# Kernel optimization log

Hardware: AMD Instinct MI355X
Metric: run time of the kernel (lower is better)

Reference implementation:

```python
import jax, jax.numpy as jnp
import numpy as np

# NSA hyperparams (match init_kwargs)
D_BLK = 64    # d: block stride
L_CMP = 64    # compression block length (== d -> non-overlapping blocks)
L_SLC = 64    # selection block length (== l_cmp == d -> P_slc = P_cmp)
BQ = 64       # block_size_q
TOPK = 16     # slc_top_k
WL, WR = 512, 0  # sliding window (left, right)


def _nsa_forward(q, k, v, w_k, b_k, w_v, b_v, w_gate, b_gate, seqlen):
    S, qh, dim = q.shape
    kv = k.shape[1]
    H = qh // kv
    b = S // seqlen          # number of equal-length packed sequences
    s = seqlen
    scale = dim ** -0.5
    f32 = jnp.float32

    # [b, s, kv, H, e]: q head g*H+h belongs to kv head g (repeat_interleave layout)
    q5 = q.reshape(b, s, kv, H, dim)
    k3 = k.reshape(b, s, kv, dim)
    v3 = v.reshape(b, s, kv, dim)

    # ---- block compression (extract_blocks + cmp_linear over block length) ----
    n_blk = s // D_BLK
    kb = k.reshape(b, n_blk, D_BLK, kv, dim)
    vb = v.reshape(b, n_blk, D_BLK, kv, dim)
    K_cmp = jnp.einsum('bntke,t->bnke', kb, w_k) + b_k[0]
    V_cmp = jnp.einsum('bntke,t->bnke', vb, w_v) + b_v[0]

    # ---- compressed attention (per sequence, fp32 softmax) ----
    sc = jnp.einsum('bqkhe,bnke->bkhqn', q5, K_cmp).astype(f32) * scale
    P = jax.nn.softmax(sc, axis=-1)
    out_cmp = jnp.einsum('bkhqn,bnke->bqkhe', P.astype(q.dtype), V_cmp)

    # ---- selection scores: pool P over q-blocks and GQA groups, then top-k ----
    nqb = s // BQ
    pooled = P.reshape(b, kv, H, nqb, BQ, n_blk).sum(axis=(2, 4))  # [b,kv,nqb,n_blk]
    idx = jax.lax.top_k(pooled, TOPK)[1]                            # [b,kv,nqb,TOPK]

    # gather selected K/V blocks (shared by all queries in a q-block / GQA group)
    kb2 = jnp.transpose(kb, (0, 3, 1, 2, 4))  # [b,kv,n_blk,l,e]
    vb2 = jnp.transpose(vb, (0, 3, 1, 2, 4))
    gather = jax.vmap(jax.vmap(lambda blocks, i: blocks[i]))
    K_sel = gather(kb2, idx)  # [b,kv,nqb,TOPK,l,e]
    V_sel = gather(vb2, idx)

    # ---- selected-block attention ----
    qblk = q5.reshape(b, nqb, BQ, kv, H, dim)
    sc2 = jnp.einsum('bnckhe,bkntle->bkhnctl', qblk, K_sel).astype(f32) * scale
    sc2 = sc2.reshape(b, kv, H, nqb, BQ, TOPK * L_SLC)
    P2 = jax.nn.softmax(sc2, axis=-1).astype(q.dtype)
    out_slc = jnp.einsum('bkhncm,bknme->bnckhe', P2,
                         V_sel.reshape(b, kv, nqb, TOPK * L_SLC, dim))
    out_slc = out_slc.reshape(b, s, kv, H, dim)

    # ---- sliding-window attention (window_size=(WL, WR), non-causal flag) ----
    sw = jnp.einsum('bikhe,bjke->bkhij', q5, k3).astype(f32) * scale
    i = jnp.arange(s)[:, None]
    j = jnp.arange(s)[None, :]
    valid = (j >= i - WL) & (j <= i + WR)
    sw = jnp.where(valid, sw, -jnp.inf)
    Pw = jax.nn.softmax(sw, axis=-1).astype(q.dtype)
    out_win = jnp.einsum('bkhij,bjke->bikhe', Pw, v3)

    # ---- gated fusion of the three branches ----
    gate = jax.nn.sigmoid(jnp.einsum('bqkhe,ec->bqkhc', q5, w_gate) + b_gate)
    out = (gate[..., 0:1] * out_cmp
           + gate[..., 1:2] * out_slc
           + gate[..., 2:3] * out_win)
    return out.reshape(S, qh, dim)


def setup_inputs() -> dict:
    key = jax.random.key(0)
    ks = jax.random.split(key, 9)
    S, qh, kvh, dim = 4096, 8, 2, 128
    inp = {
        'q': jax.random.normal(ks[0], (S, qh, dim), jnp.float32),
        'k': jax.random.normal(ks[1], (S, kvh, dim), jnp.float32),
        'v': jax.random.normal(ks[2], (S, kvh, dim), jnp.float32),
        'w_k': jax.random.normal(ks[3], (L_CMP,), jnp.float32) * (L_CMP ** -0.5),
        'b_k': jax.random.normal(ks[4], (1,), jnp.float32) * 0.02,
        'w_v': jax.random.normal(ks[5], (L_CMP,), jnp.float32) * (L_CMP ** -0.5),
        'b_v': jax.random.normal(ks[6], (1,), jnp.float32) * 0.02,
        'w_gate': jax.random.normal(ks[7], (dim, 3), jnp.float32) * (dim ** -0.5),
        'b_gate': jax.random.normal(ks[8], (3,), jnp.float32) * 0.02,
        'seqlen': 2048,
    }
    return inp


def reference(q, k, v, w_k, b_k, w_v, b_v, w_gate, b_gate, seqlen):
    return _nsa_forward(q, k, v, w_k, b_k, w_v, b_v, w_gate, b_gate, seqlen)
```

## Files before the change

kernel.cpp:

```cpp
#include <hip/hip_runtime.h>
#include <hip/hip_bf16.h>


#define SEQ   2048
#define NB    2
#define KV    2
#define NH    4
#define QH    8
#define DIM   128
#define NBLK  32
#define NQB   32
#define NTOP  16
#define SCALE 0.08838834764831845f
#define QS    36
#define RS    144
#define QP    136
#define VP    72

typedef unsigned short ushort_t;
using bf16x8 = __attribute__((ext_vector_type(8))) short;
using f32x4  = __attribute__((ext_vector_type(4))) float;

__device__ __forceinline__ unsigned pkbf(float a, float b){
  union { __hip_bfloat162 h; unsigned u; } cv;
  cv.h = __float22bfloat162_rn(make_float2(a, b));
  return cv.u;
}
__device__ __forceinline__ ushort_t f2b(float f){
  union { float f; unsigned i; } x; x.f = f;
  unsigned r = x.i + 0x7fffu + ((x.i >> 16) & 1u);
  return (ushort_t)(r >> 16);
}

__global__ __launch_bounds__(256) void prep_k(
    const float* __restrict__ k, const float* __restrict__ v,
    ushort_t* __restrict__ Kb, ushort_t* __restrict__ VT)
{
  int blk = blockIdx.x;
  int db = blk & 1, rb = (blk >> 1) & 31, bbg = blk >> 6;
  int bb = bbg >> 1, g = bbg & 1;
  int tid = threadIdx.x;
  __shared__ ushort_t T[64*VP];

  for (int jj = 0; jj < 4; ++jj){
    int i = tid + jj*256;
    int r = i >> 4, ds = i & 15;
    size_t src = ((size_t)(bb*SEQ + rb*64 + r)*KV + g)*DIM + db*64 + ds*4;
    float4 kx = *(const float4*)(k + src);
    float4 vx = *(const float4*)(v + src);
    uint2 kk; kk.x = pkbf(kx.x,kx.y); kk.y = pkbf(kx.z,kx.w);
    *(uint2*)&Kb[((size_t)bbg*SEQ + rb*64 + r)*DIM + db*64 + ds*4] = kk;
    unsigned v01 = pkbf(vx.x,vx.y), v23 = pkbf(vx.z,vx.w);
    T[(ds*4+0)*VP + r] = (ushort_t)(v01 & 0xffffu);
    T[(ds*4+1)*VP + r] = (ushort_t)(v01 >> 16);
    T[(ds*4+2)*VP + r] = (ushort_t)(v23 & 0xffffu);
    T[(ds*4+3)*VP + r] = (ushort_t)(v23 >> 16);
  }
  __syncthreads();
  for (int jj = 0; jj < 4; ++jj){
    int i = tid + jj*256;
    int d = i >> 4, seg = i & 15;
    uint2 u = *(uint2*)&T[d*VP + seg*4];
    *(uint2*)&VT[((size_t)bbg*DIM + db*64 + d)*SEQ + rb*64 + seg*4] = u;
  }
}

__global__ __launch_bounds__(256) void compress_k(
    const float* __restrict__ k, const float* __restrict__ v,
    const float* __restrict__ w_k, const float* __restrict__ b_k,
    const float* __restrict__ w_v, const float* __restrict__ b_v,
    float* __restrict__ Kc, float* __restrict__ Vc)
{
  int blk = blockIdx.x;
  int dh = blk & 1;
  int n  = (blk >> 1) & 31;
  int g  = (blk >> 6) & 1;
  int bb = blk >> 7;
  int tid = threadIdx.x;

  __shared__ float wks[64], wvs[64];
  __shared__ float accK[16][64], accV[16][64];
  if (tid < 64){ wks[tid] = w_k[tid]; wvs[tid] = w_v[tid]; }
  __syncthreads();

  int r4 = tid >> 4, dq = tid & 15;
  float4 sk = {0,0,0,0}, sv = {0,0,0,0};
  for (int rr = 0; rr < 4; ++rr){
    int row = r4*4 + rr;
    size_t off = ((size_t)(bb*SEQ + n*64 + row)*KV + g)*DIM + dh*64 + dq*4;
    float4 kx = *(const float4*)(k + off);
    float4 vx = *(const float4*)(v + off);
    float a = wks[row], b = wvs[row];
    sk.x += a*kx.x; sk.y += a*kx.y; sk.z += a*kx.z; sk.w += a*kx.w;
    sv.x += b*vx.x; sv.y += b*vx.y; sv.z += b*vx.z; sv.w += b*vx.w;
  }
  *(float4*)&accK[r4][dq*4] = sk;
  *(float4*)&accV[r4][dq*4] = sv;
  __syncthreads();
  size_t obase = ((size_t)((bb*KV+g)*NBLK + n))*DIM + dh*64;
  if (tid < 64){
    float s = 0.f;
#pragma unroll
    for (int i = 0; i < 16; ++i) s += accK[i][tid];
    Kc[obase + tid] = s + b_k[0];
  } else if (tid < 128){
    int d = tid - 64;
    float s = 0.f;
#pragma unroll
    for (int i = 0; i < 16; ++i) s += accV[i][d];
    Vc[obase + d] = s + b_v[0];
  }
}

__global__ __launch_bounds__(256) void cmp_attn_k(
    const float* __restrict__ q, const float* __restrict__ Kc,
    const float* __restrict__ Vc,
    const float* __restrict__ w_gate, const float* __restrict__ b_gate,
    float* __restrict__ pooled_part, float* __restrict__ out)
{
  int blk = blockIdx.x;
  int h  = blk & 3;
  int qb = (blk >> 2) & (NQB-1);
  int g  = (blk >> 7) & 1;
  int bb = blk >> 8;
  int tid = threadIdx.x;
  int qi = tid >> 2, c = tid & 3;

  __shared__ float Ks[32*RS];
  __shared__ float Vs[32*RS];
  __shared__ float wsum[4][NBLK];

  const float4* Ksrc = (const float4*)(Kc + (size_t)(bb*KV + g) * NBLK * DIM);
  const float4* Vsrc = (const float4*)(Vc + (size_t)(bb*KV + g) * NBLK * DIM);
  for (int i = tid; i < 1024; i += 256){
    int row = i >> 5, seg = i & 31;
    int dst = row*RS + (seg>>3)*QS + (seg&7)*4;
    ((float4*)(Ks+dst))[0] = Ksrc[i];
    ((float4*)(Vs+dst))[0] = Vsrc[i];
  }
  __syncthreads();

  int row = bb*SEQ + qb*64 + qi;
  float qv[32];
  {
    const float4* q4 = (const float4*)(q + ((size_t)row*QH + g*NH + h)*DIM + c*32);
#pragma unroll
    for (int j = 0; j < 8; ++j){
      float4 u = q4[j];
      qv[4*j+0]=u.x; qv[4*j+1]=u.y; qv[4*j+2]=u.z; qv[4*j+3]=u.w;
    }
  }

  float gp = 0.f;
#pragma unroll
  for (int d = 0; d < 32; ++d) gp += qv[d]*w_gate[(c*32+d)*3 + 0];
  gp += __shfl_xor(gp, 1); gp += __shfl_xor(gp, 2);
  float g0 = 1.f/(1.f + expf(-(gp + b_gate[0])));

  float sc[NBLK];
#pragma unroll
  for (int n = 0; n < NBLK; ++n){
    float p = 0.f;
    const float4* kr = (const float4*)(Ks + n*RS + c*QS);
#pragma unroll
    for (int j = 0; j < 8; ++j){
      float4 u = kr[j];
      p += qv[4*j+0]*u.x + qv[4*j+1]*u.y + qv[4*j+2]*u.z + qv[4*j+3]*u.w;
    }
    p += __shfl_xor(p, 1); p += __shfl_xor(p, 2);
    sc[n] = p * SCALE;
  }
  float m = sc[0];
#pragma unroll
  for (int n = 1; n < NBLK; ++n) m = fmaxf(m, sc[n]);
  float l = 0.f;
#pragma unroll
  for (int n = 0; n < NBLK; ++n){ sc[n] = expf(sc[n]-m); l += sc[n]; }
  float inv = 1.f/l;
#pragma unroll
  for (int n = 0; n < NBLK; ++n) sc[n] *= inv;

#pragma unroll
  for (int n = 0; n < NBLK; ++n){
    float t2 = sc[n];
    t2 += __shfl_xor(t2, 4); t2 += __shfl_xor(t2, 8);
    t2 += __shfl_xor(t2, 16); t2 += __shfl_xor(t2, 32);
    if ((tid & 63) == 0) wsum[tid>>6][n] = t2;
  }
  __syncthreads();
  if (tid < NBLK)
    pooled_part[(size_t)blk*NBLK + tid] =
        (wsum[0][tid]+wsum[1][tid]) + (wsum[2][tid]+wsum[3][tid]);

  float o[32];
#pragma unroll
  for (int d = 0; d < 32; ++d) o[d] = 0.f;
#pragma unroll
  for (int n = 0; n < NBLK; ++n){
    float pb = sc[n];
    const float4* vr = (const float4*)(Vs + n*RS + c*QS);
#pragma unroll
    for (int j = 0; j < 8; ++j){
      float4 u = vr[j];
      o[4*j+0] += pb*u.x; o[4*j+1] += pb*u.y;
      o[4*j+2] += pb*u.z; o[4*j+3] += pb*u.w;
    }
  }
  float* op = out + ((size_t)row*QH + g*NH + h)*DIM + c*32;
#pragma unroll
  for (int d = 0; d < 32; ++d) op[d] = g0*o[d];
}

__global__ __launch_bounds__(256, 3) void attn_k(
    const float* __restrict__ q, const ushort_t* __restrict__ Kb,
    const ushort_t* __restrict__ VT, const float* __restrict__ pp,
    const float* __restrict__ w_gate, const float* __restrict__ b_gate,
    float* __restrict__ slcbuf, float* __restrict__ out)
{
  int idx = blockIdx.x;
  int x = idx & 7, low = idx & 1, u = idx >> 3;
  int bbg = x >> 1;
  int j = u*2 + low;
  int role = j >> 7;
  int qb = (j >> 2) & 31;
  int h  = j & 3;
  int bb = bbg >> 1, g = bbg & 1;

  int tid = threadIdx.x;
  int lane = tid & 63, w = tid >> 6, quad = lane >> 4, l15 = lane & 15;

  __shared__ short Ks[64*QP];
  __shared__ short VTs[128*VP];
  __shared__ short Ps[64*VP];
  __shared__ float gbuf[64];
  __shared__ int   idxs[NTOP];

  if (role == 0 && tid < 64){
    int n = lane;
    float val = -INFINITY;
    if (n < NBLK){
      const float* p0 = pp + ((size_t)((bb*KV+g)*NQB + qb)*NH)*NBLK + n;
      val = (p0[0] + p0[NBLK]) + (p0[2*NBLK] + p0[3*NBLK]);
    }
    for (int t = 0; t < NTOP; ++t){
      float bv = val; int bi = n;
      for (int mm = 1; mm < 32; mm <<= 1){
        float ov = __shfl_xor(bv, mm);
        int   oi = __shfl_xor(bi, mm);
        if (ov > bv || (ov == bv && oi < bi)){ bv = ov; bi = oi; }
      }
      if (lane == 0) idxs[t] = bi;
      if (n == bi) val = -INFINITY;
    }
  }

  const float* qrow = q + ((size_t)(bb*SEQ + qb*64 + w*16 + l15)*QH + g*NH + h)*DIM;
  int gcol = 1 + role;
  bf16x8 qfrag[4];
  float gp = 0.f;
#pragma unroll
  for (int kc = 0; kc < 4; ++kc){
    int d0 = kc*32 + quad*8;
    float4 u0 = *(const float4*)(qrow + d0);
    float4 u1 = *(const float4*)(qrow + d0 + 4);
    float qf[8] = {u0.x,u0.y,u0.z,u0.w,u1.x,u1.y,u1.z,u1.w};
#pragma unroll
    for (int jj = 0; jj < 8; ++jj) gp += qf[jj]*w_gate[(d0+jj)*3 + gcol];
    union { unsigned uu[4]; bf16x8 v8; } tq;
    tq.uu[0] = pkbf(u0.x,u0.y); tq.uu[1] = pkbf(u0.z,u0.w);
    tq.uu[2] = pkbf(u1.x,u1.y); tq.uu[3] = pkbf(u1.z,u1.w);
    qfrag[kc] = tq.v8;
  }
  gp += __shfl_xor(gp,16); gp += __shfl_xor(gp,32);
  if (quad == 0) gbuf[w*16+l15] = 1.f/(1.f + __expf(-(gp + b_gate[gcol])));
  __syncthreads();
  float gl[4];
#pragma unroll
  for (int r = 0; r < 4; ++r) gl[r] = gbuf[w*16+quad*4+r];

  const ushort_t* kbase = Kb + (size_t)bbg*SEQ*DIM;
  const ushort_t* vtbase = VT + (size_t)bbg*DIM*SEQ;

  int kb0 = (qb >= 8) ? (qb - 8) : 0;
  int nph = (role == 0) ? NTOP : (qb - kb0 + 1);

  float m1[4], l1[4];
  f32x4 oacc[8];
  const f32x4 zero4 = {0.f,0.f,0.f,0.f};
#pragma unroll
  for (int r = 0; r < 4; ++r){ m1[r] = -INFINITY; l1[r] = 0.f; }
#pragma unroll
  for (int dt = 0; dt < 8; ++dt) oacc[dt] = zero4;

  for (int t = 0; t < nph; ++t){
    int kb = (role == 0) ? idxs[t] : (kb0 + t);
    __syncthreads();
    {
      const ushort_t* ksrc = kbase + (size_t)kb*64*DIM;
#pragma unroll
      for (int jj = 0; jj < 4; ++jj){
        int i = tid + jj*256;
        int row = i >> 4, seg = i & 15;
        uint4 uu = *(const uint4*)(ksrc + row*DIM + seg*8);
        *(uint4*)&Ks[row*QP + seg*8] = uu;
      }
      const ushort_t* vsrc = vtbase + kb*64;
#pragma unroll
      for (int jj = 0; jj < 4; ++jj){
        int i = tid + jj*256;
        int dr = i >> 3, seg = i & 7;
        uint4 uu = *(const uint4*)(vsrc + (size_t)dr*SEQ + seg*8);
        *(uint4*)&VTs[dr*VP + seg*8] = uu;
      }
    }
    __syncthreads();

    f32x4 sacc[4];
#pragma unroll
    for (int nt = 0; nt < 4; ++nt) sacc[nt] = zero4;
#pragma unroll
    for (int kc = 0; kc < 4; ++kc){
      bf16x8 a = qfrag[kc];
#pragma unroll
      for (int nt = 0; nt < 4; ++nt){
        bf16x8 b = *(bf16x8*)&Ks[(nt*16 + l15)*QP + kc*32 + quad*8];
        sacc[nt] = __builtin_amdgcn_mfma_f32_16x16x32_bf16(a, b, sacc[nt], 0, 0, 0);
      }
    }

    bool mlow  = (role == 1) && (kb == qb - 8);
    bool mhigh = (role == 1) && (kb == qb);
    float alpha[4];
#pragma unroll
    for (int r = 0; r < 4; ++r){
      int qi_local = w*16 + quad*4 + r;
      float mx = -INFINITY;
#pragma unroll
      for (int nt = 0; nt < 4; ++nt){
        int key = nt*16 + l15;
        float sv = sacc[nt][r]*SCALE;
        bool valid = (!mlow || key >= qi_local) && (!mhigh || key <= qi_local);
        sv = valid ? sv : -INFINITY;
        sacc[nt][r] = sv;
        mx = fmaxf(mx, sv);
      }
      mx = fmaxf(mx, __shfl_xor(mx,1)); mx = fmaxf(mx, __shfl_xor(mx,2));
      mx = fmaxf(mx, __shfl_xor(mx,4)); mx = fmaxf(mx, __shfl_xor(mx,8));
      float mn = fmaxf(m1[r], mx);
      alpha[r] = __expf(m1[r] - mn);
      float s0 = 0.f;
#pragma unroll
      for (int nt = 0; nt < 4; ++nt){
        float pe = __expf(sacc[nt][r] - mn);
        sacc[nt][r] = pe;
        s0 += pe;
      }
      s0 += __shfl_xor(s0,1); s0 += __shfl_xor(s0,2);
      s0 += __shfl_xor(s0,4); s0 += __shfl_xor(s0,8);
      l1[r] = l1[r]*alpha[r] + s0;
      m1[r] = mn;
    }
#pragma unroll
    for (int nt = 0; nt < 4; ++nt)
#pragma unroll
      for (int r = 0; r < 4; ++r)
        Ps[(w*16 + quad*4 + r)*VP + nt*16 + l15] = (short)f2b(sacc[nt][r]);
#pragma unroll
    for (int dt = 0; dt < 8; ++dt)
#pragma unroll
      for (int r = 0; r < 4; ++r) oacc[dt][r] *= alpha[r];
#pragma unroll
    for (int kc2 = 0; kc2 < 2; ++kc2){
      bf16x8 pa = *(bf16x8*)&Ps[(w*16 + l15)*VP + kc2*32 + quad*8];
#pragma unroll
      for (int dt = 0; dt < 8; ++dt){
        bf16x8 vb8 = *(bf16x8*)&VTs[(dt*16 + l15)*VP + kc2*32 + quad*8];
        oacc[dt] = __builtin_amdgcn_mfma_f32_16x16x32_bf16(pa, vb8, oacc[dt], 0, 0, 0);
      }
    }
  }

#pragma unroll
  for (int r = 0; r < 4; ++r){
    float s2 = gl[r] / l1[r];
    size_t ob = ((size_t)(bb*SEQ + qb*64 + w*16 + quad*4 + r)*QH + g*NH + h)*DIM + l15;
    if (role == 0){
      float* op = slcbuf + ob;
#pragma unroll
      for (int dt = 0; dt < 8; ++dt) op[dt*16] = s2 * oacc[dt][r];
    } else {
      float* op = out + ob;
#pragma unroll
      for (int dt = 0; dt < 8; ++dt) op[dt*16] += s2 * oacc[dt][r];
    }
  }
}

__global__ __launch_bounds__(256) void merge_k(const float* __restrict__ slcbuf,
                                               float* __restrict__ out){
  int i = blockIdx.x * 256 + threadIdx.x;
  float4 a = ((const float4*)slcbuf)[i];
  float4 b = ((float4*)out)[i];
  b.x += a.x; b.y += a.y; b.z += a.z; b.w += a.w;
  ((float4*)out)[i] = b;
}

extern "C" void kernel_launch(void* const* d_in, const int* in_sizes, int n_in,
                              void* d_out, int out_size, void* d_ws, size_t ws_size,
                              hipStream_t stream) {
  const float* q      = (const float*)d_in[0];
  const float* k      = (const float*)d_in[1];
  const float* v      = (const float*)d_in[2];
  const float* w_k    = (const float*)d_in[3];
  const float* b_k    = (const float*)d_in[4];
  const float* w_v    = (const float*)d_in[5];
  const float* b_v    = (const float*)d_in[6];
  const float* w_gate = (const float*)d_in[7];
  const float* b_gate = (const float*)d_in[8];
  float* out = (float*)d_out;

  float* ws     = (float*)d_ws;
  float* Kc     = ws;
  float* Vc     = ws + 16384;
  float* pp     = ws + 32768;
  float* slcbuf = ws + 49152;
  ushort_t* Kb  = (ushort_t*)(ws + 4243456);
  ushort_t* VT  = Kb + 1048576;

  prep_k    <<<256, 256, 0, stream>>>(k, v, Kb, VT);
  compress_k<<<256, 256, 0, stream>>>(k, v, w_k, b_k, w_v, b_v, Kc, Vc);
  cmp_attn_k<<<NB*KV*NQB*NH, 256, 0, stream>>>(q, Kc, Vc, w_gate, b_gate, pp, out);
  attn_k    <<<1024, 256, 0, stream>>>(q, Kb, VT, pp, w_gate, b_gate, slcbuf, out);
  merge_k   <<<4096, 256, 0, stream>>>(slcbuf, out);
}
```

Measured before the change: 199.2 us.

## Double-buffer K/V tiles with async global-to-LDS loads and swizzled layouts

The attention kernel now stages the next selected or window K/V block into a second LDS buffer using global_load_lds while the current block is computed, instead of a synchronous load-then-barrier per block. The prep kernel writes K and V^T to global memory with an XOR swizzle so the async copies land bank-conflict-free without padding. The QK MFMA operands are swapped so each lane owns one query row, which shrinks the softmax reductions to two cross-quad shuffles. Masking is skipped for unmasked blocks, and MFMA sections are wrapped in setprio. The extra LDS for double buffering lowers the occupancy target from 3 to 2 blocks per CU, which reduces latency hiding across blocks.

```diff
diff --git a/kernel.cpp b/kernel.cpp
--- a/kernel.cpp
+++ b/kernel.cpp
@@ -14,7 +14,6 @@
 #define SCALE 0.08838834764831845f
 #define QS    36
 #define RS    144
-#define QP    136
 #define VP    72
 
 typedef unsigned short ushort_t;
@@ -26,10 +25,12 @@
   cv.h = __float22bfloat162_rn(make_float2(a, b));
   return cv.u;
 }
-__device__ __forceinline__ ushort_t f2b(float f){
-  union { float f; unsigned i; } x; x.f = f;
-  unsigned r = x.i + 0x7fffu + ((x.i >> 16) & 1u);
-  return (ushort_t)(r >> 16);
+
+__device__ __forceinline__ void async16(ushort_t* l, const ushort_t* g){
+  __builtin_amdgcn_global_load_lds(
+      (const __attribute__((address_space(1))) unsigned int*)(size_t)g,
+      (__attribute__((address_space(3))) unsigned int*)(size_t)l,
+      16, 0, 0);
 }
 
 __global__ __launch_bounds__(256) void prep_k(
@@ -49,7 +50,9 @@
     float4 kx = *(const float4*)(k + src);
     float4 vx = *(const float4*)(v + src);
     uint2 kk; kk.x = pkbf(kx.x,kx.y); kk.y = pkbf(kx.z,kx.w);
-    *(uint2*)&Kb[((size_t)bbg*SEQ + rb*64 + r)*DIM + db*64 + ds*4] = kk;
+    size_t rowb = ((size_t)bbg*SEQ + rb*64 + r)*DIM*2;
+    int swz = (db*128 + ds*8) ^ ((r & 7) << 4);
+    *(uint2*)((char*)Kb + rowb + swz) = kk;
     unsigned v01 = pkbf(vx.x,vx.y), v23 = pkbf(vx.z,vx.w);
     T[(ds*4+0)*VP + r] = (ushort_t)(v01 & 0xffffu);
     T[(ds*4+1)*VP + r] = (ushort_t)(v01 >> 16);
@@ -61,7 +64,9 @@
     int i = tid + jj*256;
     int d = i >> 4, seg = i & 15;
     uint2 u = *(uint2*)&T[d*VP + seg*4];
-    *(uint2*)&VT[((size_t)bbg*DIM + db*64 + d)*SEQ + rb*64 + seg*4] = u;
+    size_t rowb = ((size_t)bbg*DIM + db*64 + d)*SEQ*2;
+    int swz = (seg*8) ^ ((d & 7) << 4);
+    *(uint2*)((char*)VT + rowb + rb*128 + swz) = u;
   }
 }
 
@@ -211,7 +216,7 @@
   for (int d = 0; d < 32; ++d) op[d] = g0*o[d];
 }
 
-__global__ __launch_bounds__(256, 3) void attn_k(
+__global__ __launch_bounds__(256, 2) void attn_k(
     const float* __restrict__ q, const ushort_t* __restrict__ Kb,
     const ushort_t* __restrict__ VT, const float* __restrict__ pp,
     const float* __restrict__ w_gate, const float* __restrict__ b_gate,
@@ -228,10 +233,11 @@
 
   int tid = threadIdx.x;
   int lane = tid & 63, w = tid >> 6, quad = lane >> 4, l15 = lane & 15;
-
-  __shared__ short Ks[64*QP];
-  __shared__ short VTs[128*VP];
-  __shared__ short Ps[64*VP];
+  int xr = (l15 & 7) << 4;
+
+  __shared__ ushort_t Ks[2][64*128];
+  __shared__ ushort_t VTs[2][128*64];
+  __shared__ ushort_t Ps[64*VP];
   __shared__ float gbuf[64];
   __shared__ int   idxs[NTOP];
 
@@ -278,111 +284,141 @@
 #pragma unroll
   for (int r = 0; r < 4; ++r) gl[r] = gbuf[w*16+quad*4+r];
 
-  const ushort_t* kbase = Kb + (size_t)bbg*SEQ*DIM;
+  const ushort_t* kbase  = Kb + (size_t)bbg*SEQ*DIM;
   const ushort_t* vtbase = VT + (size_t)bbg*DIM*SEQ;
 
   int kb0 = (qb >= 8) ? (qb - 8) : 0;
   int nph = (role == 0) ? NTOP : (qb - kb0 + 1);
-
-  float m1[4], l1[4];
+  int qi_local = w*16 + l15;
+
+  float m1 = -INFINITY, l1 = 0.f;
   f32x4 oacc[8];
   const f32x4 zero4 = {0.f,0.f,0.f,0.f};
 #pragma unroll
-  for (int r = 0; r < 4; ++r){ m1[r] = -INFINITY; l1[r] = 0.f; }
-#pragma unroll
   for (int dt = 0; dt < 8; ++dt) oacc[dt] = zero4;
 
+  auto stage = [&](int bufi, int kb_){
+    const ushort_t* ksrc = kbase + (size_t)kb_*64*DIM;
+#pragma unroll
+    for (int jj = 0; jj < 4; ++jj){
+      int i = tid + jj*256;
+      async16(&Ks[bufi][(jj*256 + w*64)*8], ksrc + (size_t)i*8);
+    }
+    const ushort_t* vsrc = vtbase + kb_*64;
+#pragma unroll
+    for (int jj = 0; jj < 4; ++jj){
+      int i = tid + jj*256;
+      int d = i >> 3, sg = i & 7;
+      async16(&VTs[bufi][(jj*256 + w*64)*8], vsrc + (size_t)d*SEQ + sg*8);
+    }
+  };
+
+  stage(0, (role == 0) ? idxs[0] : kb0);
+
   for (int t = 0; t < nph; ++t){
+    int cur = t & 1;
     int kb = (role == 0) ? idxs[t] : (kb0 + t);
     __syncthreads();
-    {
-      const ushort_t* ksrc = kbase + (size_t)kb*64*DIM;
-#pragma unroll
-      for (int jj = 0; jj < 4; ++jj){
-        int i = tid + jj*256;
-        int row = i >> 4, seg = i & 15;
-        uint4 uu = *(const uint4*)(ksrc + row*DIM + seg*8);
-        *(uint4*)&Ks[row*QP + seg*8] = uu;
-      }
-      const ushort_t* vsrc = vtbase + kb*64;
-#pragma unroll
-      for (int jj = 0; jj < 4; ++jj){
-        int i = tid + jj*256;
-        int dr = i >> 3, seg = i & 7;
-        uint4 uu = *(const uint4*)(vsrc + (size_t)dr*SEQ + seg*8);
-        *(uint4*)&VTs[dr*VP + seg*8] = uu;
-      }
-    }
-    __syncthreads();
+    if (t+1 < nph){
+      int kbn = (role == 0) ? idxs[t+1] : (kb0 + t + 1);
+      stage(cur ^ 1, kbn);
+    }
+    __builtin_amdgcn_sched_barrier(0);
 
     f32x4 sacc[4];
 #pragma unroll
     for (int nt = 0; nt < 4; ++nt) sacc[nt] = zero4;
+    __builtin_amdgcn_s_setprio(1);
 #pragma unroll
     for (int kc = 0; kc < 4; ++kc){
-      bf16x8 a = qfrag[kc];
+      bf16x8 b = qfrag[kc];
 #pragma unroll
       for (int nt = 0; nt < 4; ++nt){
-        bf16x8 b = *(bf16x8*)&Ks[(nt*16 + l15)*QP + kc*32 + quad*8];
+        bf16x8 a = *(bf16x8*)((char*)&Ks[cur][0] + (nt*16 + l15)*256
+                              + ((kc*64 + quad*16) ^ xr));
         sacc[nt] = __builtin_amdgcn_mfma_f32_16x16x32_bf16(a, b, sacc[nt], 0, 0, 0);
       }
     }
+    __builtin_amdgcn_s_setprio(0);
 
     bool mlow  = (role == 1) && (kb == qb - 8);
     bool mhigh = (role == 1) && (kb == qb);
-    float alpha[4];
-#pragma unroll
-    for (int r = 0; r < 4; ++r){
-      int qi_local = w*16 + quad*4 + r;
-      float mx = -INFINITY;
-#pragma unroll
-      for (int nt = 0; nt < 4; ++nt){
-        int key = nt*16 + l15;
-        float sv = sacc[nt][r]*SCALE;
-        bool valid = (!mlow || key >= qi_local) && (!mhigh || key <= qi_local);
-        sv = valid ? sv : -INFINITY;
-        sacc[nt][r] = sv;
-        mx = fmaxf(mx, sv);
-      }
-      mx = fmaxf(mx, __shfl_xor(mx,1)); mx = fmaxf(mx, __shfl_xor(mx,2));
-      mx = fmaxf(mx, __shfl_xor(mx,4)); mx = fmaxf(mx, __shfl_xor(mx,8));
-      float mn = fmaxf(m1[r], mx);
-      alpha[r] = __expf(m1[r] - mn);
-      float s0 = 0.f;
-#pragma unroll
-      for (int nt = 0; nt < 4; ++nt){
+    float mx = -INFINITY;
+    if (mlow | mhigh){
+#pragma unroll
+      for (int nt = 0; nt < 4; ++nt)
+#pragma unroll
+        for (int r = 0; r < 4; ++r){
+          int key = nt*16 + quad*4 + r;
+          float sv = sacc[nt][r]*SCALE;
+          bool valid = (!mlow || key >= qi_local) && (!mhigh || key <= qi_local);
+          sv = valid ? sv : -INFINITY;
+          sacc[nt][r] = sv;
+          mx = fmaxf(mx, sv);
+        }
+    } else {
+#pragma unroll
+      for (int nt = 0; nt < 4; ++nt)
+#pragma unroll
+        for (int r = 0; r < 4; ++r){
+          float sv = sacc[nt][r]*SCALE;
+          sacc[nt][r] = sv;
+          mx = fmaxf(mx, sv);
+        }
+    }
+    mx = fmaxf(mx, __shfl_xor(mx, 16));
+    mx = fmaxf(mx, __shfl_xor(mx, 32));
+    float mn = fmaxf(m1, mx);
+    float al = __expf(m1 - mn);
+    float s0 = 0.f;
+#pragma unroll
+    for (int nt = 0; nt < 4; ++nt)
+#pragma unroll
+      for (int r = 0; r < 4; ++r){
         float pe = __expf(sacc[nt][r] - mn);
         sacc[nt][r] = pe;
         s0 += pe;
       }
-      s0 += __shfl_xor(s0,1); s0 += __shfl_xor(s0,2);
-      s0 += __shfl_xor(s0,4); s0 += __shfl_xor(s0,8);
-      l1[r] = l1[r]*alpha[r] + s0;
-      m1[r] = mn;
-    }
-#pragma unroll
-    for (int nt = 0; nt < 4; ++nt)
-#pragma unroll
-      for (int r = 0; r < 4; ++r)
-        Ps[(w*16 + quad*4 + r)*VP + nt*16 + l15] = (short)f2b(sacc[nt][r]);
+    s0 += __shfl_xor(s0, 16);
+    s0 += __shfl_xor(s0, 32);
+    l1 = l1*al + s0;
+    m1 = mn;
+
+#pragma unroll
+    for (int nt = 0; nt < 4; ++nt){
+      uint2 pk;
+      pk.x = pkbf(sacc[nt][0], sacc[nt][1]);
+      pk.y = pkbf(sacc[nt][2], sacc[nt][3]);
+      *(uint2*)&Ps[(w*16 + l15)*VP + nt*16 + quad*4] = pk;
+    }
+
+    float ar[4];
+#pragma unroll
+    for (int r = 0; r < 4; ++r) ar[r] = __shfl(al, quad*4 + r);
 #pragma unroll
     for (int dt = 0; dt < 8; ++dt)
 #pragma unroll
-      for (int r = 0; r < 4; ++r) oacc[dt][r] *= alpha[r];
+      for (int r = 0; r < 4; ++r) oacc[dt][r] *= ar[r];
 #pragma unroll
     for (int kc2 = 0; kc2 < 2; ++kc2){
       bf16x8 pa = *(bf16x8*)&Ps[(w*16 + l15)*VP + kc2*32 + quad*8];
+      __builtin_amdgcn_s_setprio(1);
 #pragma unroll
       for (int dt = 0; dt < 8; ++dt){
-        bf16x8 vb8 = *(bf16x8*)&VTs[(dt*16 + l15)*VP + kc2*32 + quad*8];
+        bf16x8 vb8 = *(bf16x8*)((char*)&VTs[cur][0] + (dt*16 + l15)*128
+                                + ((kc2*64 + quad*16) ^ xr));
         oacc[dt] = __builtin_amdgcn_mfma_f32_16x16x32_bf16(pa, vb8, oacc[dt], 0, 0, 0);
       }
-    }
-  }
-
+      __builtin_amdgcn_s_setprio(0);
+    }
+  }
+
+  float lr[4];
+#pragma unroll
+  for (int r = 0; r < 4; ++r) lr[r] = __shfl(l1, quad*4 + r);
 #pragma unroll
   for (int r = 0; r < 4; ++r){
-    float s2 = gl[r] / l1[r];
+    float s2 = gl[r] / lr[r];
     size_t ob = ((size_t)(bb*SEQ + qb*64 + w*16 + quad*4 + r)*QH + g*NH + h)*DIM + l15;
     if (role == 0){
       float* op = slcbuf + ob;
```

Result: faster. 186.4 us (-6.4%).
